# Kernel tuning notes

Measured on AMD Instinct MI355X. Metric: run time of the kernel, lower is better.

Reference implementation:

```python
import jax, jax.numpy as jnp
import numpy as np

USER_NUM = 100000
ITEM_NUM = 50000
D = 64
E = 3200000
B = 16384


def setup_inputs() -> dict:
    key = jax.random.key(0)
    ks = jax.random.split(key, 12)
    user = jax.random.randint(ks[0], (B,), 0, USER_NUM)
    item_i = jax.random.randint(ks[1], (B,), 0, ITEM_NUM)
    item_j = jax.random.randint(ks[2], (B,), 0, ITEM_NUM)
    edge_u = jax.random.randint(ks[3], (E,), 0, USER_NUM)
    edge_i = jax.random.randint(ks[4], (E,), 0, ITEM_NUM)
    edge_val = jax.random.uniform(ks[5], (E,), dtype=jnp.float32)
    # nn.init.normal_(std=0.01)
    user_emb = 0.01 * jax.random.normal(ks[6], (USER_NUM, D), dtype=jnp.float32)
    item_emb = 0.01 * jax.random.normal(ks[7], (ITEM_NUM, D), dtype=jnp.float32)
    old_U_emb = 0.01 * jax.random.normal(ks[8], (USER_NUM, D), dtype=jnp.float32)
    old_I_emb = 0.01 * jax.random.normal(ks[9], (ITEM_NUM, D), dtype=jnp.float32)
    n_U = jax.random.uniform(ks[10], (USER_NUM,), dtype=jnp.float32)
    n_U = n_U / jnp.linalg.norm(n_U)  # pre_self normalizes by L2 norm
    n_I = jax.random.uniform(ks[11], (ITEM_NUM,), dtype=jnp.float32)
    n_I = n_I / jnp.linalg.norm(n_I)
    return {"user": user, "item_i": item_i, "item_j": item_j,
            "edge_u": edge_u, "edge_i": edge_i, "edge_val": edge_val,
            "user_emb": user_emb, "item_emb": item_emb,
            "old_U_emb": old_U_emb, "old_I_emb": old_I_emb,
            "n_U": n_U, "n_I": n_I}


def _spmm(seg_ids, gather_ids, vals, x, num_segments):
    # one hop of sparse adjacency @ dense embeddings: gather -> scale -> scatter-add
    msg = vals[:, None] * x[gather_ids]          # [E, D]
    return jax.ops.segment_sum(msg, seg_ids, num_segments=num_segments)


def reference(user, item_i, item_j, edge_u, edge_i, edge_val,
              user_emb, item_emb, old_U_emb, old_I_emb, n_U, n_I):
    # 3-hop LightGCN-style propagation over bipartite graph
    g1u = _spmm(edge_u, edge_i, edge_val, item_emb, USER_NUM)
    g1i = _spmm(edge_i, edge_u, edge_val, user_emb, ITEM_NUM)
    g2u = _spmm(edge_u, edge_i, edge_val, g1i, USER_NUM)
    g2i = _spmm(edge_i, edge_u, edge_val, g1u, ITEM_NUM)
    g3u = _spmm(edge_u, edge_i, edge_val, g2i, USER_NUM)
    g3i = _spmm(edge_i, edge_u, edge_val, g2u, ITEM_NUM)
    gcn_u = user_emb + 0.5 * g1u + (1.0 / 3.0) * g2u + 0.25 * g3u
    gcn_i = item_emb + 0.5 * g1i + (1.0 / 3.0) * g2i + 0.25 * g3i

    # BPR loss
    u = gcn_u[user]
    ii = gcn_i[item_i]
    ij = gcn_i[item_j]
    pred_i = jnp.sum(u * ii, axis=-1)
    pred_j = jnp.sum(u * ij, axis=-1)
    bpr = -jnp.mean(jax.nn.log_sigmoid(pred_i - pred_j))
    reg = 1e-4 * jnp.mean(jnp.sum(u ** 2 + ii ** 2 + ij ** 2, axis=-1))
    loss_bpr = bpr + reg

    # self-distillation loss (loss_self)
    Ud = jnp.linalg.norm(old_U_emb - gcn_u, axis=1)  # [USER_NUM]
    Id = jnp.linalg.norm(old_I_emb - gcn_i, axis=1)  # [ITEM_NUM]
    loss_self = jnp.dot(Ud, n_U) / USER_NUM + jnp.dot(Id, n_I) / ITEM_NUM

    return jnp.stack([loss_bpr, 100.0 * loss_self,
                      jnp.float32(1.0), jnp.float32(1.0)])
```

## Files before the change

### kernel.cpp

```cpp
#include <hip/hip_runtime.h>

#define USER_NUM 100000
#define ITEM_NUM 50000
#define DD 64
#define NEDGE 3200000
#define NB 16384
#define NSLOT 256

#define ATILE 4096
#define NTILE ((NEDGE + ATILE - 1) / ATILE)
#define USH 9
#define ISH 8
#define UBK ((USER_NUM + (1 << USH) - 1) >> USH)
#define IBK ((ITEM_NUM + (1 << ISH) - 1) >> ISH)
#define NBK (UBK + IBK)
#define CPAD 16
#define HIST_GRID 784
#define UHALF (USER_NUM / 2)
#define BCAP 18432

#define FP8_SCALE 64.0f

typedef float v2f __attribute__((ext_vector_type(2)));

__device__ __forceinline__ float waveReduceSum(float x) {
#pragma unroll
    for (int off = 32; off > 0; off >>= 1)
        x += __shfl_down(x, off, 64);
    return x;
}

__device__ __forceinline__ unsigned roundbf(unsigned y) {
    return (y + 0x7fffu + ((y >> 16) & 1u)) >> 16;
}

__device__ __forceinline__ void dec8(const uint2 b, float* f) {
    v2f f0 = __builtin_amdgcn_cvt_pk_f32_fp8(b.x, false);
    v2f f1 = __builtin_amdgcn_cvt_pk_f32_fp8(b.x, true);
    v2f f2 = __builtin_amdgcn_cvt_pk_f32_fp8(b.y, false);
    v2f f3 = __builtin_amdgcn_cvt_pk_f32_fp8(b.y, true);
    f[0] = f0.x; f[1] = f0.y; f[2] = f1.x; f[3] = f1.y;
    f[4] = f2.x; f[5] = f2.y; f[6] = f3.x; f[7] = f3.y;
}
__device__ __forceinline__ void fma8p(const uint2 b, const float v, v2f* a) {
    v2f f0 = __builtin_amdgcn_cvt_pk_f32_fp8(b.x, false);
    v2f f1 = __builtin_amdgcn_cvt_pk_f32_fp8(b.x, true);
    v2f f2 = __builtin_amdgcn_cvt_pk_f32_fp8(b.y, false);
    v2f f3 = __builtin_amdgcn_cvt_pk_f32_fp8(b.y, true);
    const v2f vv = {v, v};
    a[0] += vv * f0;
    a[1] += vv * f1;
    a[2] += vv * f2;
    a[3] += vv * f3;
}
__device__ __forceinline__ uint2 pack_fp8x8(const float* a) {
    int lo = 0, hi = 0;
    lo = __builtin_amdgcn_cvt_pk_fp8_f32(a[0], a[1], lo, false);
    lo = __builtin_amdgcn_cvt_pk_fp8_f32(a[2], a[3], lo, true);
    hi = __builtin_amdgcn_cvt_pk_fp8_f32(a[4], a[5], hi, false);
    hi = __builtin_amdgcn_cvt_pk_fp8_f32(a[6], a[7], hi, true);
    return make_uint2((unsigned)lo, (unsigned)hi);
}

__global__ void __launch_bounds__(256) cvt8_kernel(
    const float4* __restrict__ src, uint2* __restrict__ dst, int n8) {
    int t = blockIdx.x * blockDim.x + threadIdx.x;
    if (t < n8) {
        float4 a = src[2 * t], b = src[2 * t + 1];
        float f[8] = {a.x * FP8_SCALE, a.y * FP8_SCALE, a.z * FP8_SCALE, a.w * FP8_SCALE,
                      b.x * FP8_SCALE, b.y * FP8_SCALE, b.z * FP8_SCALE, b.w * FP8_SCALE};
        dst[t] = pack_fp8x8(f);
    }
}


__global__ void __launch_bounds__(256) coarse_hist(
    const int4* __restrict__ eu4, const int4* __restrict__ ei4,
    int* __restrict__ coarseCnt) {
    __shared__ int lc[NBK];
    const int t = threadIdx.x;
    for (int j = t; j < NBK; j += 256) lc[j] = 0;
    __syncthreads();
    for (int k = blockIdx.x * 256 + t; k < NEDGE / 4; k += HIST_GRID * 256) {
        int4 u = eu4[k];
        int4 i = ei4[k];
        atomicAdd(&lc[u.x >> USH], 1); atomicAdd(&lc[u.y >> USH], 1);
        atomicAdd(&lc[u.z >> USH], 1); atomicAdd(&lc[u.w >> USH], 1);
        atomicAdd(&lc[UBK + (i.x >> ISH)], 1); atomicAdd(&lc[UBK + (i.y >> ISH)], 1);
        atomicAdd(&lc[UBK + (i.z >> ISH)], 1); atomicAdd(&lc[UBK + (i.w >> ISH)], 1);
    }
    __syncthreads();
    for (int j = t; j < NBK; j += 256)
        if (lc[j]) atomicAdd(&coarseCnt[j * CPAD], lc[j]);
}

__global__ void __launch_bounds__(512) coarse_scan(
    const int* __restrict__ cnt, int* __restrict__ base, int* __restrict__ cur) {
    __shared__ int a[512];
    const int t = threadIdx.x;
    int v = (t < UBK) ? cnt[t * CPAD] : 0;
    a[t] = v;
    __syncthreads();
    for (int off = 1; off < 512; off <<= 1) {
        int x = (t >= off) ? a[t - off] : 0;
        __syncthreads();
        a[t] += x;
        __syncthreads();
    }
    if (t < UBK) { base[t] = a[t] - v; cur[t * CPAD] = a[t] - v; }
    __syncthreads();
    v = (t < IBK) ? cnt[(UBK + t) * CPAD] : 0;
    a[t] = v;
    __syncthreads();
    for (int off = 1; off < 512; off <<= 1) {
        int x = (t >= off) ? a[t - off] : 0;
        __syncthreads();
        a[t] += x;
        __syncthreads();
    }
    if (t < IBK) { base[UBK + t] = a[t] - v; cur[(UBK + t) * CPAD] = a[t] - v; }
}

__global__ void __launch_bounds__(256, 4) binA(
    const int* __restrict__ eu, const int* __restrict__ ei,
    const float* __restrict__ ev,
    int* __restrict__ ccur,
    int2* __restrict__ stU, int2* __restrict__ stI) {
    __shared__ int2 pay[ATILE];
    __shared__ unsigned char sbid[ATILE];
    __shared__ int hist[256];
    __shared__ int pscan[256];
    __shared__ int cursor[256];
    __shared__ int delta[256];

    const int t = threadIdx.x;
    const int dirI = blockIdx.y;
    const int tb = blockIdx.x * ATILE;
    const int n = min(ATILE, NEDGE - tb);
    const int* key = dirI ? ei : eu;
    const int SH = dirI ? ISH : USH;

    hist[t] = 0;
    __syncthreads();
    for (int k = t; k < n; k += 256)
        atomicAdd(&hist[key[tb + k] >> SH], 1);
    __syncthreads();
    pscan[t] = hist[t];
    __syncthreads();
    for (int off = 1; off < 256; off <<= 1) {
        int x = (t >= off) ? pscan[t - off] : 0;
        __syncthreads();
        pscan[t] += x;
        __syncthreads();
    }
    {
        const int c = hist[t];
        const int lst = pscan[t] - c;
        cursor[t] = lst;
        int gp = 0;
        if (c > 0) {
            int* gc = dirI ? (ccur + UBK * CPAD) : ccur;
            gp = atomicAdd(&gc[t * CPAD], c);
        }
        delta[t] = gp - lst;
    }
    __syncthreads();
    if (dirI == 0) {
        for (int k = t; k < n; k += 256) {
            const int e = tb + k;
            const int u = eu[e], i = ei[e];
            const int b = u >> USH;
            const int p = atomicAdd(&cursor[b], 1);
            pay[p] = make_int2(((u & ((1 << USH) - 1)) << 16) | i,
                               __float_as_int(ev[e]));
            sbid[p] = (unsigned char)b;
        }
    } else {
        for (int k = t; k < n; k += 256) {
            const int e = tb + k;
            const int u = eu[e], i = ei[e];
            const int b = i >> ISH;
            const int p = atomicAdd(&cursor[b], 1);
            pay[p] = make_int2(((i & ((1 << ISH) - 1)) << 17) | u,
                               __float_as_int(ev[e]));
            sbid[p] = (unsigned char)b;
        }
    }
    __syncthreads();
    int2* st = dirI ? stI : stU;
    for (int p = t; p < n; p += 256)
        st[delta[sbid[p]] + p] = pay[p];
}

__global__ void __launch_bounds__(256) binB(
    const int2* __restrict__ stU, const int2* __restrict__ stI,
    const int* __restrict__ base, const int* __restrict__ cnt,
    int* __restrict__ rpU, int* __restrict__ rpI, int* __restrict__ rpIm,
    unsigned* __restrict__ ivU, unsigned* __restrict__ ivI) {
    __shared__ int h[512];
    __shared__ unsigned pay[BCAP];
    const int t = threadIdx.x;
    const int b = blockIdx.x;
    if (b < UBK) {
        const int s = base[b], n = cnt[b * CPAD];
        const int dbase = b << USH;
        h[t] = 0; h[t + 256] = 0;
        __syncthreads();
        for (int p = s + t; p < s + n; p += 256)
            atomicAdd(&h[(unsigned)stU[p].x >> 16], 1);
        __syncthreads();
        const int o0 = h[t], o1 = h[t + 256];
        for (int off = 1; off < 512; off <<= 1) {
            int x0 = (t >= off) ? h[t - off] : 0;
            int x1 = (t + 256 >= off) ? h[t + 256 - off] : 0;
            __syncthreads();
            h[t] += x0; h[t + 256] += x1;
            __syncthreads();
        }
        const int e0 = h[t] - o0, e1 = h[t + 256] - o1;
        __syncthreads();
        h[t] = e0; h[t + 256] = e1;
        if (dbase + t < USER_NUM) rpU[dbase + t] = s + e0;
        if (dbase + 256 + t < USER_NUM) rpU[dbase + 256 + t] = s + e1;
        if (t == 0 && dbase + 512 >= USER_NUM) rpU[USER_NUM] = s + n;
        __syncthreads();
        if (n <= BCAP) {
            for (int p = s + t; p < s + n; p += 256) {
                int2 en = stU[p];
                unsigned x = (unsigned)en.x;
                int pos = atomicAdd(&h[x >> 16], 1);
                unsigned bf = roundbf((unsigned)en.y);
                pay[pos] = (bf << 16) | (x & 0xFFFFu);
            }
            __syncthreads();
            for (int k = t; k < n; k += 256) ivU[s + k] = pay[k];
        } else {
            for (int p = s + t; p < s + n; p += 256) {
                int2 en = stU[p];
                unsigned x = (unsigned)en.x;
                int pos = atomicAdd(&h[x >> 16], 1);
                unsigned bf = roundbf((unsigned)en.y);
                ivU[s + pos] = (bf << 16) | (x & 0xFFFFu);
            }
        }
    } else {
        const int ib = b - UBK;
        const int s = base[b], n = cnt[b * CPAD];
        const int dbase = ib << ISH;
        h[t] = 0; h[t + 256] = 0;
        __syncthreads();
        for (int p = s + t; p < s + n; p += 256) {
            unsigned x = (unsigned)stI[p].x;
            const int c = (int)((x >> 17) << 1) | (((x & 0x1FFFFu) >= UHALF) ? 1 : 0);
            atomicAdd(&h[c], 1);
        }
        __syncthreads();
        const int c0 = h[2 * t], c1 = h[2 * t + 1];
        for (int off = 1; off < 512; off <<= 1) {
            int x0 = (t >= off) ? h[t - off] : 0;
            int x1 = (t + 256 >= off) ? h[t + 256 - off] : 0;
            __syncthreads();
            h[t] += x0; h[t + 256] += x1;
            __syncthreads();
        }
        const int incl0 = h[2 * t], incl1 = h[2 * t + 1];
        const int st0 = incl0 - c0;
        const int st1 = incl1 - c1;
        __syncthreads();
        h[2 * t] = st0; h[2 * t + 1] = st1;
        if (dbase + t < ITEM_NUM) { rpI[dbase + t] = s + st0; rpIm[dbase + t] = s + st1; }
        if (t == 0 && dbase + 256 >= ITEM_NUM) rpI[ITEM_NUM] = s + n;
        __syncthreads();
        if (n <= BCAP) {
            for (int p = s + t; p < s + n; p += 256) {
                int2 en = stI[p];
                unsigned x = (unsigned)en.x;
                const int c = (int)((x >> 17) << 1) | (((x & 0x1FFFFu) >= UHALF) ? 1 : 0);
                int pos = atomicAdd(&h[c], 1);
                unsigned v15 = roundbf((unsigned)en.y) & 0x7FFFu;
                pay[pos] = (v15 << 17) | (x & 0x1FFFFu);
            }
            __syncthreads();
            for (int k = t; k < n; k += 256) ivI[s + k] = pay[k];
        } else {
            for (int p = s + t; p < s + n; p += 256) {
                int2 en = stI[p];
                unsigned x = (unsigned)en.x;
                const int c = (int)((x >> 17) << 1) | (((x & 0x1FFFFu) >= UHALF) ? 1 : 0);
                int pos = atomicAdd(&h[c], 1);
                unsigned v15 = roundbf((unsigned)en.y) & 0x7FFFu;
                ivI[s + pos] = (v15 << 17) | (x & 0x1FFFFu);
            }
        }
    }
}

#define UW (USER_NUM / 8)
#define IW (ITEM_NUM / 8)

template<bool ISU>
__device__ __forceinline__ int xof(unsigned q) {
    return ISU ? (int)(q & 0xFFFFu) : (int)(q & 0x1FFFFu);
}
template<bool ISU>
__device__ __forceinline__ float vof(unsigned q) {
    return ISU ? __uint_as_float(q & 0xFFFF0000u)
               : __uint_as_float((q >> 17) << 16);
}

template<bool ISU, int N>
__device__ __forceinline__ void edge_block(
    const unsigned* __restrict__ iv, int t,
    const uint2* __restrict__ srcr, v2f* a0, v2f* a1) {
    unsigned q[N];
    uint2 b[N];
#pragma unroll
    for (int j = 0; j < N; j++) q[j] = iv[t + j];
#pragma unroll
    for (int j = 0; j < N; j++) b[j] = srcr[xof<ISU>(q[j]) * 8];
#pragma unroll
    for (int j = 0; j < N; j++) fma8p(b[j], vof<ISU>(q[j]), (j & 1) ? a1 : a0);
}

template<bool ISU>
__device__ __forceinline__ void accum_range(
    const unsigned* __restrict__ iv, const uint2* __restrict__ srcr,
    int s, int e2, v2f* a0, v2f* a1) {
    int t = s;
    for (; t + 15 < e2; t += 16) edge_block<ISU, 16>(iv, t, srcr, a0, a1);
    if (t + 7 < e2) { edge_block<ISU, 8>(iv, t, srcr, a0, a1); t += 8; }
    if (t + 3 < e2) { edge_block<ISU, 4>(iv, t, srcr, a0, a1); t += 4; }
    if (t + 1 < e2) { edge_block<ISU, 2>(iv, t, srcr, a0, a1); t += 2; }
    if (t < e2)     edge_block<ISU, 1>(iv, t, srcr, a0, a1);
}

__device__ __forceinline__ void acc_combine(const v2f* a0, const v2f* a1, float* acc) {
#pragma unroll
    for (int k = 0; k < 4; k++) {
        const v2f sv = a0[k] + a1[k];
        acc[2 * k]     = sv.x;
        acc[2 * k + 1] = sv.y;
    }
}

__device__ __forceinline__ void row_accum_u(
    const int* __restrict__ rp, const unsigned* __restrict__ iv,
    const uint2* __restrict__ src, int row, int r, float* acc) {
    v2f a0[4] = {{0.f, 0.f}, {0.f, 0.f}, {0.f, 0.f}, {0.f, 0.f}};
    v2f a1[4] = {{0.f, 0.f}, {0.f, 0.f}, {0.f, 0.f}, {0.f, 0.f}};
    accum_range<true>(iv, src + r, rp[row], rp[row + 1], a0, a1);
    acc_combine(a0, a1, acc);
}

__device__ __forceinline__ void row_accum_i(
    const int* __restrict__ rp, const int* __restrict__ rpm,
    const unsigned* __restrict__ iv,
    const uint2* __restrict__ src, int row, int r, float* acc) {
    v2f a0[4] = {{0.f, 0.f}, {0.f, 0.f}, {0.f, 0.f}, {0.f, 0.f}};
    v2f a1[4] = {{0.f, 0.f}, {0.f, 0.f}, {0.f, 0.f}, {0.f, 0.f}};
    const int s = rp[row], m = rpm[row], e = rp[row + 1];
    accum_range<false>(iv, src + r, s, m, a0, a1);
    accum_range<false>(iv, src + r, m, e, a0, a1);
    acc_combine(a0, a1, acc);
}

__global__ void __launch_bounds__(256) gather_hop_f8(
    const int* __restrict__ rpU, const unsigned* __restrict__ ivU,
    const uint2* __restrict__ srcForU, uint2* __restrict__ outU,
    const int* __restrict__ rpI, const int* __restrict__ rpIm,
    const unsigned* __restrict__ ivI,
    const uint2* __restrict__ srcForI, uint2* __restrict__ outI) {
    const int lane = threadIdx.x & 63;
    const int sub = lane >> 3;
    const int r = lane & 7;
    const int wave = blockIdx.x * 4 + (threadIdx.x >> 6);
    float acc[8];
    if (wave < UW) {
        const int row = wave * 8 + sub;
        row_accum_u(rpU, ivU, srcForU, row, r, acc);
        outU[row * 8 + r] = pack_fp8x8(acc);
    } else if (wave < UW + IW) {
        const int row = (wave - UW) * 8 + sub;
        row_accum_i(rpI, rpIm, ivI, srcForI, row, r, acc);
        outI[row * 8 + r] = pack_fp8x8(acc);
    }
}

__global__ void __launch_bounds__(256) gather_hop3(
    const int* __restrict__ rpU, const unsigned* __restrict__ ivU,
    const uint2* __restrict__ srcForU,
    const int* __restrict__ rpI, const int* __restrict__ rpIm,
    const unsigned* __restrict__ ivI, const uint2* __restrict__ srcForI,
    const float4* __restrict__ embU, const uint2* __restrict__ g1u,
    const uint2* __restrict__ g2u, float4* __restrict__ gcnU,
    const float4* __restrict__ embI, const uint2* __restrict__ g1i,
    const uint2* __restrict__ g2i, float4* __restrict__ gcnI,
    const float4* __restrict__ oldU4, const float4* __restrict__ oldI4,
    const float* __restrict__ nU, const float* __restrict__ nI,
    float* __restrict__ accs) {
    const int lane = threadIdx.x & 63;
    const int sub = lane >> 3;
    const int r = lane & 7;
    const int wave = blockIdx.x * 4 + (threadIdx.x >> 6);
    float acc[8];
    const float4* emb; const uint2* g1; const uint2* g2; float4* gcn; int row;
    const float4* old4; const float* nrm; bool isU;
    if (wave < UW) {
        row = wave * 8 + sub;
        row_accum_u(rpU, ivU, srcForU, row, r, acc);
        emb = embU; g1 = g1u; g2 = g2u; gcn = gcnU;
        old4 = oldU4; nrm = nU; isU = true;
    } else if (wave < UW + IW) {
        row = (wave - UW) * 8 + sub;
        row_accum_i(rpI, rpIm, ivI, srcForI, row, r, acc);
        emb = embI; g1 = g1i; g2 = g2i; gcn = gcnI;
        old4 = oldI4; nrm = nI; isU = false;
    } else return;
    {
        const float C1 = 0.5f / FP8_SCALE;
        const float C2 = (1.0f / 3.0f) / FP8_SCALE;
        const float C3 = 0.25f / FP8_SCALE;
        float f1[8], f2[8];
        dec8(g1[row * 8 + r], f1);
        dec8(g2[row * 8 + r], f2);
        const float4 e0 = emb[row * 16 + 2 * r];
        const float4 e1 = emb[row * 16 + 2 * r + 1];
        float4 o0, o1;
        o0.x = e0.x + C1 * f1[0] + C2 * f2[0] + C3 * acc[0];
        o0.y = e0.y + C1 * f1[1] + C2 * f2[1] + C3 * acc[1];
        o0.z = e0.z + C1 * f1[2] + C2 * f2[2] + C3 * acc[2];
        o0.w = e0.w + C1 * f1[3] + C2 * f2[3] + C3 * acc[3];
        o1.x = e1.x + C1 * f1[4] + C2 * f2[4] + C3 * acc[4];
        o1.y = e1.y + C1 * f1[5] + C2 * f2[5] + C3 * acc[5];
        o1.z = e1.z + C1 * f1[6] + C2 * f2[6] + C3 * acc[6];
        o1.w = e1.w + C1 * f1[7] + C2 * f2[7] + C3 * acc[7];
        gcn[row * 16 + 2 * r] = o0;
        gcn[row * 16 + 2 * r + 1] = o1;
        const float4 d0 = old4[row * 16 + 2 * r];
        const float4 d1 = old4[row * 16 + 2 * r + 1];
        const float ex = d0.x - o0.x, ey = d0.y - o0.y;
        const float ez = d0.z - o0.z, ew = d0.w - o0.w;
        const float fx = d1.x - o1.x, fy = d1.y - o1.y;
        const float fz = d1.z - o1.z, fw = d1.w - o1.w;
        float ss = ex * ex + ey * ey + ez * ez + ew * ew
                 + fx * fx + fy * fy + fz * fz + fw * fw;
        ss += __shfl_xor(ss, 1, 64);
        ss += __shfl_xor(ss, 2, 64);
        ss += __shfl_xor(ss, 4, 64);
        float val = (r == 0) ? sqrtf(ss) * nrm[row] : 0.0f;
        val = waveReduceSum(val);
        if (lane == 0) {
            const int slot = wave & (NSLOT - 1);
            unsafeAtomicAdd(&accs[(isU ? 2 : 3) * NSLOT + slot], val);
        }
    }
}

__global__ void __launch_bounds__(256) bpr_loss(
    const int* __restrict__ user, const int* __restrict__ itemI,
    const int* __restrict__ itemJ,
    const float4* __restrict__ gcnU4, const float4* __restrict__ gcnI4,
    float* __restrict__ accs) {
    const int lane = threadIdx.x & 63;
    const int sub = lane >> 4;
    const int r = lane & 15;
    const int W = blockIdx.x * 4 + (threadIdx.x >> 6);
    const int NW = gridDim.x * 4;
    float accB = 0.0f, accR = 0.0f;
    for (int g = W; g < NB / 4; g += NW) {
        const int samp = g * 4 + sub;
        const int uu = user[samp], vi = itemI[samp], vj = itemJ[samp];
        const float4 u  = gcnU4[uu * 16 + r];
        const float4 xi = gcnI4[vi * 16 + r];
        const float4 xj = gcnI4[vj * 16 + r];
        float pi = u.x * xi.x + u.y * xi.y + u.z * xi.z + u.w * xi.w;
        float pj = u.x * xj.x + u.y * xj.y + u.z * xj.z + u.w * xj.w;
        float rg = u.x * u.x + u.y * u.y + u.z * u.z + u.w * u.w
                 + xi.x * xi.x + xi.y * xi.y + xi.z * xi.z + xi.w * xi.w
                 + xj.x * xj.x + xj.y * xj.y + xj.z * xj.z + xj.w * xj.w;
#pragma unroll
        for (int off = 1; off <= 8; off <<= 1) {
            pi += __shfl_xor(pi, off, 64);
            pj += __shfl_xor(pj, off, 64);
            rg += __shfl_xor(rg, off, 64);
        }
        if (r == 0) {
            const float x = pi - pj;
            accB += fmaxf(-x, 0.0f) + log1pf(expf(-fabsf(x)));
            accR += rg;
        }
    }
    accB = waveReduceSum(accB);
    accR = waveReduceSum(accR);
    if (lane == 0) {
        const int slot = W & (NSLOT - 1);
        unsafeAtomicAdd(&accs[0 * NSLOT + slot], accB);
        unsafeAtomicAdd(&accs[1 * NSLOT + slot], accR);
    }
}

__global__ void __launch_bounds__(64) finalize(const float* __restrict__ accs,
                                               float* __restrict__ out) {
    const int lane = threadIdx.x;
    float s[4];
#pragma unroll
    for (int k = 0; k < 4; k++) {
        float v = 0.0f;
        for (int j = lane; j < NSLOT; j += 64) v += accs[k * NSLOT + j];
        s[k] = waveReduceSum(v);
    }
    if (lane == 0) {
        const float loss_bpr = s[0] / NB + 1e-4f * (s[1] / NB);
        const float loss_self = s[2] / USER_NUM + s[3] / ITEM_NUM;
        out[0] = loss_bpr;
        out[1] = 100.0f * loss_self;
        out[2] = 1.0f;
        out[3] = 1.0f;
    }
}

extern "C" void kernel_launch(void* const* d_in, const int* in_sizes, int n_in,
                              void* d_out, int out_size, void* d_ws, size_t ws_size,
                              hipStream_t stream) {
    const int*   user     = (const int*)d_in[0];
    const int*   item_i   = (const int*)d_in[1];
    const int*   item_j   = (const int*)d_in[2];
    const int*   edge_u   = (const int*)d_in[3];
    const int*   edge_i   = (const int*)d_in[4];
    const float* edge_val = (const float*)d_in[5];
    const float* user_emb = (const float*)d_in[6];
    const float* item_emb = (const float*)d_in[7];
    const float* old_U    = (const float*)d_in[8];
    const float* old_I    = (const float*)d_in[9];
    const float* n_U      = (const float*)d_in[10];
    const float* n_I      = (const float*)d_in[11];
    float* out = (float*)d_out;

    char* base = (char*)d_ws;
    size_t off = 0;
    auto carve = [&](size_t bytes) {
        char* p = base + off;
        off += (bytes + 255) & ~(size_t)255;
        return p;
    };
    int*      coarseCnt = (int*)carve(NBK * CPAD * 4);
    float*    accs      = (float*)carve(4 * NSLOT * 4);
    size_t zero_bytes = off;
    int*      cbase = (int*)carve(NBK * 4);
    int*      ccur  = (int*)carve(NBK * CPAD * 4);
    int*      rpU   = (int*)carve((USER_NUM + 1) * 4);
    int*      rpI   = (int*)carve((ITEM_NUM + 1) * 4);
    int*      rpIm  = (int*)carve((ITEM_NUM + 1) * 4);
    unsigned* ivU   = (unsigned*)carve((size_t)NEDGE * 4);
    unsigned* ivI   = (unsigned*)carve((size_t)NEDGE * 4);
    uint2*    ebU8  = (uint2*)carve((size_t)USER_NUM * DD);
    uint2*    ebI8  = (uint2*)carve((size_t)ITEM_NUM * DD);
    uint2*    g1u8  = (uint2*)carve((size_t)USER_NUM * DD);
    uint2*    g1i8  = (uint2*)carve((size_t)ITEM_NUM * DD);
    uint2*    g2u8  = (uint2*)carve((size_t)USER_NUM * DD);
    uint2*    g2i8  = (uint2*)carve((size_t)ITEM_NUM * DD);
    int2*     stU   = (int2*)carve((size_t)NEDGE * 8);
    int2*     stI   = (int2*)carve((size_t)NEDGE * 8);
    float* gcnU = (float*)stU;
    float* gcnI = (float*)stI;

    hipMemsetAsync(d_ws, 0, zero_bytes, stream);

    const dim3 blk(256);

    cvt8_kernel<<<(USER_NUM * 8 + 255) / 256, blk, 0, stream>>>(
        (const float4*)user_emb, ebU8, USER_NUM * 8);
    cvt8_kernel<<<(ITEM_NUM * 8 + 255) / 256, blk, 0, stream>>>(
        (const float4*)item_emb, ebI8, ITEM_NUM * 8);

    coarse_hist<<<HIST_GRID, blk, 0, stream>>>((const int4*)edge_u,
                                               (const int4*)edge_i, coarseCnt);
    coarse_scan<<<1, 512, 0, stream>>>(coarseCnt, cbase, ccur);
    binA<<<dim3(NTILE, 2), blk, 0, stream>>>(edge_u, edge_i, edge_val,
                                             ccur, stU, stI);
    binB<<<NBK, blk, 0, stream>>>(stU, stI, cbase, coarseCnt,
                                  rpU, rpI, rpIm, ivU, ivI);

    const int hop_waves = UW + IW;
    const int hop_grid = (hop_waves + 3) / 4;

    gather_hop_f8<<<hop_grid, blk, 0, stream>>>(rpU, ivU, ebI8, g1u8,
                                                rpI, rpIm, ivI, ebU8, g1i8);
    gather_hop_f8<<<hop_grid, blk, 0, stream>>>(rpU, ivU, g1i8, g2u8,
                                                rpI, rpIm, ivI, g1u8, g2i8);
    gather_hop3<<<hop_grid, blk, 0, stream>>>(
        rpU, ivU, g2i8, rpI, rpIm, ivI, g2u8,
        (const float4*)user_emb, g1u8, g2u8, (float4*)gcnU,
        (const float4*)item_emb, g1i8, g2i8, (float4*)gcnI,
        (const float4*)old_U, (const float4*)old_I, n_U, n_I, accs);

    bpr_loss<<<128, blk, 0, stream>>>(user, item_i, item_j,
                                      (const float4*)gcnU, (const float4*)gcnI, accs);
    finalize<<<1, 64, 0, stream>>>(accs, out);
}
```

Measured before the change: 506.3 us.

## Stage per-wave edge index lists in LDS and schedule item rows first

Each wave now cooperatively loads the contiguous edge index range for its 8 rows into a per-wave shared memory buffer. The gather loops then read indices from LDS instead of global memory, falling back to global when the range exceeds the buffer capacity. Item rows are now assigned to the lower wave ids and user rows after them, which changes the work order. The cost is an extra staging pass, a block-wide barrier and 16KB of LDS per block, which may lower occupancy.

```diff
diff --git a/kernel.cpp b/kernel.cpp
--- a/kernel.cpp
+++ b/kernel.cpp
@@ -18,6 +18,7 @@
 #define HIST_GRID 784
 #define UHALF (USER_NUM / 2)
 #define BCAP 18432
+#define IVCAP 1024
 
 #define FP8_SCALE 64.0f
 
@@ -343,47 +344,62 @@
     }
 }
 
-__device__ __forceinline__ void row_accum_u(
-    const int* __restrict__ rp, const unsigned* __restrict__ iv,
-    const uint2* __restrict__ src, int row, int r, float* acc) {
-    v2f a0[4] = {{0.f, 0.f}, {0.f, 0.f}, {0.f, 0.f}, {0.f, 0.f}};
-    v2f a1[4] = {{0.f, 0.f}, {0.f, 0.f}, {0.f, 0.f}, {0.f, 0.f}};
-    accum_range<true>(iv, src + r, rp[row], rp[row + 1], a0, a1);
-    acc_combine(a0, a1, acc);
-}
-
-__device__ __forceinline__ void row_accum_i(
-    const int* __restrict__ rp, const int* __restrict__ rpm,
-    const unsigned* __restrict__ iv,
-    const uint2* __restrict__ src, int row, int r, float* acc) {
-    v2f a0[4] = {{0.f, 0.f}, {0.f, 0.f}, {0.f, 0.f}, {0.f, 0.f}};
-    v2f a1[4] = {{0.f, 0.f}, {0.f, 0.f}, {0.f, 0.f}, {0.f, 0.f}};
-    const int s = rp[row], m = rpm[row], e = rp[row + 1];
-    accum_range<false>(iv, src + r, s, m, a0, a1);
-    accum_range<false>(iv, src + r, m, e, a0, a1);
-    acc_combine(a0, a1, acc);
-}
-
 __global__ void __launch_bounds__(256) gather_hop_f8(
     const int* __restrict__ rpU, const unsigned* __restrict__ ivU,
     const uint2* __restrict__ srcForU, uint2* __restrict__ outU,
     const int* __restrict__ rpI, const int* __restrict__ rpIm,
     const unsigned* __restrict__ ivI,
     const uint2* __restrict__ srcForI, uint2* __restrict__ outI) {
+    __shared__ unsigned sIv[4][IVCAP];
+    const int wslot = threadIdx.x >> 6;
     const int lane = threadIdx.x & 63;
     const int sub = lane >> 3;
     const int r = lane & 7;
-    const int wave = blockIdx.x * 4 + (threadIdx.x >> 6);
+    const int wave = blockIdx.x * 4 + wslot;
+    const bool active = wave < UW + IW;
+    const bool isI = wave < IW;
+    int rowBase = 0;
+    const int* rp = rpU; const unsigned* ivg = ivU;
+    if (active) {
+        rowBase = isI ? wave * 8 : (wave - IW) * 8;
+        rp  = isI ? rpI : rpU;
+        ivg = isI ? ivI : ivU;
+    }
+    int sB = 0, eB = 0;
+    if (active) { sB = rp[rowBase]; eB = rp[rowBase + 8]; }
+    unsigned* buf = sIv[wslot];
+    const int nst = min(eB - sB, IVCAP);
+    for (int k = lane; k < nst; k += 64) buf[k] = ivg[sB + k];
+    __syncthreads();
+    if (!active) return;
+    const int row = rowBase + sub;
+    const int sr = rp[row], er = rp[row + 1];
     float acc[8];
-    if (wave < UW) {
-        const int row = wave * 8 + sub;
-        row_accum_u(rpU, ivU, srcForU, row, r, acc);
-        outU[row * 8 + r] = pack_fp8x8(acc);
-    } else if (wave < UW + IW) {
-        const int row = (wave - UW) * 8 + sub;
-        row_accum_i(rpI, rpIm, ivI, srcForI, row, r, acc);
-        outI[row * 8 + r] = pack_fp8x8(acc);
-    }
+    v2f a0[4] = {{0.f,0.f},{0.f,0.f},{0.f,0.f},{0.f,0.f}};
+    v2f a1[4] = {{0.f,0.f},{0.f,0.f},{0.f,0.f},{0.f,0.f}};
+    if (eB - sB <= IVCAP) {
+        const unsigned* p = buf - sB;
+        if (isI) {
+            const int mr = rpIm[row];
+            const uint2* srcr = srcForI + r;
+            accum_range<false>(p, srcr, sr, mr, a0, a1);
+            accum_range<false>(p, srcr, mr, er, a0, a1);
+        } else {
+            accum_range<true>(p, srcForU + r, sr, er, a0, a1);
+        }
+    } else {
+        if (isI) {
+            const int mr = rpIm[row];
+            const uint2* srcr = srcForI + r;
+            accum_range<false>(ivg, srcr, sr, mr, a0, a1);
+            accum_range<false>(ivg, srcr, mr, er, a0, a1);
+        } else {
+            accum_range<true>(ivg, srcForU + r, sr, er, a0, a1);
+        }
+    }
+    acc_combine(a0, a1, acc);
+    if (isI) outI[row * 8 + r] = pack_fp8x8(acc);
+    else     outU[row * 8 + r] = pack_fp8x8(acc);
 }
 
 __global__ void __launch_bounds__(256) gather_hop3(
@@ -398,28 +414,64 @@
     const float4* __restrict__ oldU4, const float4* __restrict__ oldI4,
     const float* __restrict__ nU, const float* __restrict__ nI,
     float* __restrict__ accs) {
+    __shared__ unsigned sIv[4][IVCAP];
+    const int wslot = threadIdx.x >> 6;
     const int lane = threadIdx.x & 63;
     const int sub = lane >> 3;
     const int r = lane & 7;
-    const int wave = blockIdx.x * 4 + (threadIdx.x >> 6);
+    const int wave = blockIdx.x * 4 + wslot;
+    const bool active = wave < UW + IW;
+    const bool isI = wave < IW;
+    int rowBase = 0;
+    const int* rp = rpU; const unsigned* ivg = ivU;
+    if (active) {
+        rowBase = isI ? wave * 8 : (wave - IW) * 8;
+        rp  = isI ? rpI : rpU;
+        ivg = isI ? ivI : ivU;
+    }
+    int sB = 0, eB = 0;
+    if (active) { sB = rp[rowBase]; eB = rp[rowBase + 8]; }
+    unsigned* buf = sIv[wslot];
+    const int nst = min(eB - sB, IVCAP);
+    for (int k = lane; k < nst; k += 64) buf[k] = ivg[sB + k];
+    __syncthreads();
+    if (!active) return;
+    const int row = rowBase + sub;
+    const int sr = rp[row], er = rp[row + 1];
     float acc[8];
-    const float4* emb; const uint2* g1; const uint2* g2; float4* gcn; int row;
-    const float4* old4; const float* nrm; bool isU;
-    if (wave < UW) {
-        row = wave * 8 + sub;
-        row_accum_u(rpU, ivU, srcForU, row, r, acc);
-        emb = embU; g1 = g1u; g2 = g2u; gcn = gcnU;
-        old4 = oldU4; nrm = nU; isU = true;
-    } else if (wave < UW + IW) {
-        row = (wave - UW) * 8 + sub;
-        row_accum_i(rpI, rpIm, ivI, srcForI, row, r, acc);
-        emb = embI; g1 = g1i; g2 = g2i; gcn = gcnI;
-        old4 = oldI4; nrm = nI; isU = false;
-    } else return;
+    v2f a0[4] = {{0.f,0.f},{0.f,0.f},{0.f,0.f},{0.f,0.f}};
+    v2f a1[4] = {{0.f,0.f},{0.f,0.f},{0.f,0.f},{0.f,0.f}};
+    if (eB - sB <= IVCAP) {
+        const unsigned* p = buf - sB;
+        if (isI) {
+            const int mr = rpIm[row];
+            const uint2* srcr = srcForI + r;
+            accum_range<false>(p, srcr, sr, mr, a0, a1);
+            accum_range<false>(p, srcr, mr, er, a0, a1);
+        } else {
+            accum_range<true>(p, srcForU + r, sr, er, a0, a1);
+        }
+    } else {
+        if (isI) {
+            const int mr = rpIm[row];
+            const uint2* srcr = srcForI + r;
+            accum_range<false>(ivg, srcr, sr, mr, a0, a1);
+            accum_range<false>(ivg, srcr, mr, er, a0, a1);
+        } else {
+            accum_range<true>(ivg, srcForU + r, sr, er, a0, a1);
+        }
+    }
+    acc_combine(a0, a1, acc);
     {
         const float C1 = 0.5f / FP8_SCALE;
         const float C2 = (1.0f / 3.0f) / FP8_SCALE;
         const float C3 = 0.25f / FP8_SCALE;
+        const float4* emb  = isI ? embI : embU;
+        const uint2*  g1   = isI ? g1i  : g1u;
+        const uint2*  g2   = isI ? g2i  : g2u;
+        float4*       gcn  = isI ? gcnI : gcnU;
+        const float4* old4 = isI ? oldI4 : oldU4;
+        const float*  nrm  = isI ? nI   : nU;
         float f1[8], f2[8];
         dec8(g1[row * 8 + r], f1);
         dec8(g2[row * 8 + r], f2);
@@ -451,7 +503,7 @@
         val = waveReduceSum(val);
         if (lane == 0) {
             const int slot = wave & (NSLOT - 1);
-            unsafeAtomicAdd(&accs[(isU ? 2 : 3) * NSLOT + slot], val);
+            unsafeAtomicAdd(&accs[(isI ? 3 : 2) * NSLOT + slot], val);
         }
     }
 }
```

Result: faster. 480.7 us, median of 2 (-5.0%).
